# Optimization experiments

Hardware: AMD Instinct MI355X
Metric: run time of the kernel (lower is better)

## Reference

```python
import jax, jax.numpy as jnp
import numpy as np

B, H, W = 32, 64, 64
D = 8        # input_dim (capsule dim of incoming caps)
C = 8        # input_ch (number of incoming capsule types)
DIM = 8      # dim_capsule (output capsule dim)
NCH = 8      # n_channels (number of output capsule types)


def _gconv(x, w, groups, stride=1):
    # x: NHWC, w: HWIO with I = in_ch/groups, O = total out (grouped by output blocks)
    return jax.lax.conv_general_dilated(
        x, w, (stride, stride), 'SAME',
        dimension_numbers=('NHWC', 'HWIO', 'NHWC'),
        feature_group_count=groups)


def setup_inputs():
    key = jax.random.key(0)
    ks = jax.random.split(key, 5)
    inputs = jax.random.normal(ks[0], (B, H, W, D, C), jnp.float32)
    Att_W = jax.random.normal(ks[1], (1, 1, DIM, C, C * NCH), jnp.float32) * 0.05
    ConvTrans_W = jax.random.normal(ks[2], (3, 3, D, C * DIM * NCH), jnp.float32) * 0.05
    ConvTrans_B = jnp.zeros((C * DIM * NCH,), jnp.float32)
    FeaExt_W = jax.random.normal(ks[3], (3, 3, DIM, DIM * NCH), jnp.float32) * 0.05
    FeaExt_B = jnp.zeros((DIM * NCH,), jnp.float32)
    CapsAct_W = jax.random.normal(ks[4], (1, 1, DIM, DIM * NCH), jnp.float32) * 0.05
    CapsAct_B = jnp.zeros((DIM * NCH,), jnp.float32)
    return {'inputs': inputs, 'Att_W': Att_W, 'ConvTrans_W': ConvTrans_W,
            'ConvTrans_B': ConvTrans_B, 'FeaExt_W': FeaExt_W, 'FeaExt_B': FeaExt_B,
            'CapsAct_W': CapsAct_W, 'CapsAct_B': CapsAct_B}


def reference(inputs, Att_W, ConvTrans_W, ConvTrans_B, FeaExt_W, FeaExt_B,
              CapsAct_W, CapsAct_B):
    # --- ConvTrans: per input-capsule-type 3x3 conv (== grouped conv over C groups) ---
    # inputs [B,H,W,D,C] -> [B,H,W,C*D] with group-major ordering
    xt = jnp.transpose(inputs, (0, 1, 2, 4, 3)).reshape(B, H, W, C * D)
    # ConvTrans_W [3,3,D, C*DIM*NCH]: output block i is the kernel for input group i
    y = _gconv(xt, ConvTrans_W, groups=C) + ConvTrans_B  # [B,H,W, C*DIM*NCH]
    # -> u[b,h,w,d,c_in,n]  (matches concat+transpose in the original)
    u = y.reshape(B, H, W, C, DIM, NCH).transpose(0, 1, 2, 4, 3, 5)

    # --- Attention: conv3d with kernel [1,1,DIM,C,C] per output type n (VALID over DIM) ---
    # Att_W [1,1,DIM,C,C*NCH] -> A[d, c_in, n, c_out]
    A = Att_W[0, 0].reshape(DIM, C, NCH, C)
    att = jnp.einsum('bhwdcn,dcno->bhwon', u, A)       # [B,H,W,C,NCH]
    att = jax.nn.softmax(att, axis=3)                  # softmax over input_ch
    v = jnp.einsum('bhwdon,bhwon->bhwdn', u, att)      # weighted sum over input_ch

    # --- FeaExt (3x3, grouped over NCH) + ReLU, then CapsAct (1x1, grouped) ---
    vt = jnp.transpose(v, (0, 1, 2, 4, 3)).reshape(B, H, W, NCH * DIM)
    h1 = jax.nn.relu(_gconv(vt, FeaExt_W, groups=NCH) + FeaExt_B)
    h2 = _gconv(h1, CapsAct_W, groups=NCH) + CapsAct_B
    out = h2.reshape(B, H, W, NCH, DIM).transpose(0, 1, 2, 4, 3)  # [B,H,W,DIM,NCH]
    return out
```

## Files before the change

kernel.cpp:

```cpp
#include <hip/hip_runtime.h>
#include <hip/hip_fp16.h>

#define HH 64
#define WW 64

typedef short bf16x8 __attribute__((ext_vector_type(8)));
typedef float f32x4 __attribute__((ext_vector_type(4)));
typedef unsigned short u16x8 __attribute__((ext_vector_type(8)));

#define FWREP_OFF 0
#define CWREP_OFF 4608
#define LBIAS_OFF 5120
#define M1REP_OFF 5184
#define BUREP_OFF 29760
#define VT_OFF    54336
#define PREP_N    103488

__device__ __forceinline__ unsigned short f2bf(float x) {
  unsigned int u = __float_as_uint(x);
  return (unsigned short)((u + 0x7FFFu + ((u >> 16) & 1u)) >> 16);
}
__device__ __forceinline__ unsigned short f2h(float x) {
  return __half_as_ushort(__float2half(x));
}

union F4H8 { float4 f4; __half h[8]; };

__global__ __launch_bounds__(256) void prep_kernel(
    const float* __restrict__ attw, const float* __restrict__ ctw,
    const float* __restrict__ ctb, const float* __restrict__ few,
    const float* __restrict__ caw, float* __restrict__ ws) {
  int i = blockIdx.x * 256 + threadIdx.x;
  if (i >= PREP_N) return;
  if (i < 4608) {
    int e = i & 63, slot = e >> 3, j = e & 7;
    int k = (i >> 6) % 9, n = i / 576;
    int d = 2 * (slot & 3) + (slot >> 2);
    ws[FWREP_OFF + i] = few[(k * 8 + d) * 64 + n * 8 + j];
  } else if (i < 5120) {
    int z = i - 4608;
    int j = z & 7, d = (z >> 3) & 7, n = (z >> 6) & 7;
    ws[CWREP_OFF + z] = caw[d * 64 + n * 8 + j];
  } else if (i < 5184) {
    int col = i - 5120;
    int s = col >> 4, l15 = col & 15;
    int o = 2 * s + (l15 >> 3), n = l15 & 7;
    float acc = 0.f;
    for (int c = 0; c < 8; ++c)
      for (int d = 0; d < 8; ++d)
        acc += ctb[c * 64 + d * 8 + n] * attw[d * 512 + c * 64 + n * 8 + o];
    ws[LBIAS_OFF + col] = acc;
  } else if (i < 5184 + 49152) {
    int z = i - 5184;
    int j = z & 7, lane = (z >> 3) & 63, s = (z >> 9) & 3;
    int rc = z >> 11, r = rc % 3, c = rc / 3;
    int q = lane >> 4, l15 = lane & 15;
    int t = r * 4 + q, dd = j;
    int o = 2 * s + (l15 >> 3), n = l15 & 7;
    float acc = 0.f;
    if (t < 9)
      for (int d = 0; d < 8; ++d)
        acc += ctw[(t * 8 + dd) * 512 + c * 64 + d * 8 + n] *
               attw[d * 512 + c * 64 + n * 8 + o];
    ((unsigned short*)(ws + M1REP_OFF))[z] = f2bf(acc);
  } else {
    int z = i - 5184 - 49152;
    int j = z & 7, lane = (z >> 3) & 63, s = (z >> 9) & 3;
    int rc = z >> 11, r = rc % 3, c = rc / 3;
    int q = lane >> 4, l15 = lane & 15;
    int t = r * 4 + q, dd = j;
    int d = 2 * s + (l15 >> 3), n = l15 & 7;
    float val = (t < 9) ? ctw[(t * 8 + dd) * 512 + c * 64 + d * 8 + n] : 0.f;
    ((unsigned short*)(ws + BUREP_OFF))[z] = f2bf(val);
  }
}

__global__ __launch_bounds__(256, 2) void caps_stage1(
    const float* __restrict__ in, const float* __restrict__ ws,
    const float* __restrict__ ctb, __half* __restrict__ vt) {
  __shared__ unsigned short xt[181 * 72];
  __shared__ unsigned short attb[128 * 72];
  int bid = blockIdx.x;
  int b = bid >> 5;
  int t5 = bid & 31;
  int ty = t5 >> 3, tx = t5 & 7;
  int tid = threadIdx.x;

  for (int i = tid; i < 181 * 8; i += 256) {
    int c = i & 7, hp = i >> 3;
    float xs[8] = {0.f, 0.f, 0.f, 0.f, 0.f, 0.f, 0.f, 0.f};
    if (hp < 180) {
      int hy = hp / 10, hx = hp - hy * 10;
      int gy = ty * 16 + hy - 1, gx = tx * 8 + hx - 1;
      if (gy >= 0 && gy < HH && gx >= 0 && gx < WW) {
        const float* src = in + (((b * HH + gy) * WW + gx) * 64 + c);
#pragma unroll
        for (int d = 0; d < 8; ++d) xs[d] = src[d * 8];
      }
    }
    u16x8 pk;
#pragma unroll
    for (int d = 0; d < 8; ++d) pk[d] = f2bf(xs[d]);
    *(u16x8*)&xt[hp * 72 + c * 8] = pk;
  }
  __syncthreads();

  int w = __builtin_amdgcn_readfirstlane(tid >> 6);
  int lane = tid & 63;
  int q = lane >> 4, l15 = lane & 15;
  int h = l15 >> 3, n = l15 & 7;

  int hpt[2][3];
#pragma unroll
  for (int i2 = 0; i2 < 2; ++i2) {
    int pyA = (2 * w + i2) * 2 + h;
    int pxA = l15 & 7;
#pragma unroll
    for (int r = 0; r < 3; ++r) {
      int t = r * 4 + q;
      int hp;
      if (t < 9) {
        int ky = t / 3, kx = t - ky * 3;
        hp = (pyA + ky) * 10 + pxA + kx;
      } else {
        hp = 180;
      }
      hpt[i2][r] = hp * 72;
    }
  }

  const bf16x8* m1v = (const bf16x8*)(ws + M1REP_OFF);
  const bf16x8* buv = (const bf16x8*)(ws + BUREP_OFF);
  const float* lb = ws + LBIAS_OFF;

  f32x4 L[2][4];
#pragma unroll
  for (int s = 0; s < 4; ++s) {
    float v0 = lb[s * 16 + l15];
    L[0][s] = (f32x4){v0, v0, v0, v0};
    L[1][s] = (f32x4){v0, v0, v0, v0};
  }
#pragma unroll 1
  for (int c = 0; c < 8; ++c) {
    bf16x8 bm[12];
#pragma unroll
    for (int rs = 0; rs < 12; ++rs) bm[rs] = m1v[(c * 12 + rs) * 64 + lane];
    bf16x8 a[2][3];
#pragma unroll
    for (int i2 = 0; i2 < 2; ++i2)
#pragma unroll
      for (int r = 0; r < 3; ++r)
        a[i2][r] = *(const bf16x8*)&xt[hpt[i2][r] + c * 8];
#pragma unroll
    for (int i2 = 0; i2 < 2; ++i2)
#pragma unroll
      for (int s = 0; s < 4; ++s)
#pragma unroll
        for (int r = 0; r < 3; ++r)
          L[i2][s] = __builtin_amdgcn_mfma_f32_16x16x32_bf16(
              a[i2][r], bm[r * 4 + s], L[i2][s], 0, 0, 0);
  }

#pragma unroll
  for (int i2 = 0; i2 < 2; ++i2) {
    int pbase = (2 * w + i2) * 16 + q * 4;
#pragma unroll
    for (int r = 0; r < 4; ++r) {
      float v0 = L[i2][0][r], v1 = L[i2][1][r], v2 = L[i2][2][r], v3 = L[i2][3][r];
      float pm = fmaxf(fmaxf(v0, v1), fmaxf(v2, v3));
      float m = fmaxf(pm, __shfl_xor(pm, 8));
      float e0 = __expf(v0 - m), e1 = __expf(v1 - m);
      float e2 = __expf(v2 - m), e3 = __expf(v3 - m);
      float ps = e0 + e1 + e2 + e3;
      float inv = 1.f / (ps + __shfl_xor(ps, 8));
      int ab = (pbase + r) * 72 + n * 8 + h;
      attb[ab + 0] = f2h(e0 * inv);
      attb[ab + 2] = f2h(e1 * inv);
      attb[ab + 4] = f2h(e2 * inv);
      attb[ab + 6] = f2h(e3 * inv);
    }
  }
  __syncthreads();

  u16x8 atp[2][4];
#pragma unroll
  for (int i2 = 0; i2 < 2; ++i2)
#pragma unroll
    for (int r = 0; r < 4; ++r)
      atp[i2][r] = *(const u16x8*)&attb[((2 * w + i2) * 16 + q * 4 + r) * 72 + n * 8];

  f32x4 V[2][4];
#pragma unroll
  for (int s = 0; s < 4; ++s) {
    V[0][s] = (f32x4){0.f, 0.f, 0.f, 0.f};
    V[1][s] = (f32x4){0.f, 0.f, 0.f, 0.f};
  }
#pragma unroll 1
  for (int c = 0; c < 8; ++c) {
    bf16x8 bu[12];
#pragma unroll
    for (int rs = 0; rs < 12; ++rs) bu[rs] = buv[(c * 12 + rs) * 64 + lane];
    bf16x8 a[2][3];
#pragma unroll
    for (int i2 = 0; i2 < 2; ++i2)
#pragma unroll
      for (int r = 0; r < 3; ++r)
        a[i2][r] = *(const bf16x8*)&xt[hpt[i2][r] + c * 8];
    f32x4 U[2][4];
#pragma unroll
    for (int s = 0; s < 4; ++s) {
      float bv = ctb[c * 64 + s * 16 + l15];
      U[0][s] = (f32x4){bv, bv, bv, bv};
      U[1][s] = (f32x4){bv, bv, bv, bv};
    }
#pragma unroll
    for (int i2 = 0; i2 < 2; ++i2)
#pragma unroll
      for (int s = 0; s < 4; ++s)
#pragma unroll
        for (int r = 0; r < 3; ++r)
          U[i2][s] = __builtin_amdgcn_mfma_f32_16x16x32_bf16(
              a[i2][r], bu[r * 4 + s], U[i2][s], 0, 0, 0);
#pragma unroll
    for (int i2 = 0; i2 < 2; ++i2)
#pragma unroll
      for (int r = 0; r < 4; ++r) {
        float af = __half2float(__ushort_as_half(atp[i2][r][c]));
#pragma unroll
        for (int s = 0; s < 4; ++s) V[i2][s][r] += U[i2][s][r] * af;
      }
  }

#pragma unroll
  for (int i2 = 0; i2 < 2; ++i2)
#pragma unroll
    for (int r = 0; r < 4; ++r) {
      int p = (2 * w + i2) * 16 + q * 4 + r;
      int gy = ty * 16 + (p >> 3), gx = tx * 8 + (p & 7);
      size_t gp = (size_t)((b * HH + gy) * WW + gx);
      short4 st;
      st.x = (short)f2h(V[i2][0][r]);
      st.y = (short)f2h(V[i2][1][r]);
      st.z = (short)f2h(V[i2][2][r]);
      st.w = (short)f2h(V[i2][3][r]);
      *(short4*)((char*)vt + gp * 128 + n * 16 + h * 8) = st;
    }
}

__global__ __launch_bounds__(512, 6) void caps_stage2(
    const __half* __restrict__ vt, const float* __restrict__ ws,
    const float* __restrict__ fb, const float* __restrict__ cab,
    float* __restrict__ out) {
  __shared__ float smem[64 * 68];
  int bid = blockIdx.x;
  int b = bid >> 6;
  int t = bid & 63;
  int ty = t >> 3, tx = t & 7;
  int y0 = ty * 8 - 1, x0 = tx * 8 - 1;
  int tid = threadIdx.x;

  float4* ht = (float4*)smem;
  for (int i = tid; i < 800; i += 512) {
    int p = i >> 3, q = i & 7;
    int py = p / 10, px = p % 10;
    int gy = y0 + py, gx = x0 + px;
    float4 val = make_float4(0.f, 0.f, 0.f, 0.f);
    if (gy >= 0 && gy < HH && gx >= 0 && gx < WW)
      val = ((const float4*)(vt + ((b * HH + gy) * WW + gx) * 64))[q];
    ht[p * 8 + ((q + p) & 7)] = val;
  }
  __syncthreads();

  int n = __builtin_amdgcn_readfirstlane(tid >> 6);
  int lane = tid & 63;
  int py = lane >> 3, px = lane & 7;
  int p0 = py * 10 + px;
  const float* fwrep = ws + FWREP_OFF;
  const float* cwrep = ws + CWREP_OFF;

  float h1[8];
#pragma unroll
  for (int j = 0; j < 8; ++j) h1[j] = fb[n * 8 + j];

#pragma unroll 1
  for (int k = 0; k < 9; ++k) {
    int kh = k / 3, kw = k % 3;
    int pk = p0 + kh * 10 + kw;
    const float* wp = fwrep + (n * 9 + k) * 64;
    F4H8 xu;
    xu.f4 = ht[pk * 8 + ((n + pk) & 7)];
#pragma unroll
    for (int d = 0; d < 8; ++d) {
      float xv = __half2float(xu.h[d]);
#pragma unroll
      for (int j = 0; j < 8; ++j)
        h1[j] = fmaf(xv, wp[d * 8 + j], h1[j]);
    }
  }
#pragma unroll
  for (int j = 0; j < 8; ++j) h1[j] = fmaxf(h1[j], 0.f);

  float h2[8];
#pragma unroll
  for (int j = 0; j < 8; ++j) h2[j] = cab[n * 8 + j];
#pragma unroll
  for (int d = 0; d < 8; ++d)
#pragma unroll
    for (int j = 0; j < 8; ++j)
      h2[j] = fmaf(h1[d], cwrep[n * 64 + d * 8 + j], h2[j]);

  __syncthreads();
#pragma unroll
  for (int j = 0; j < 8; ++j) {
    int mch = 2 * j + (n >> 2);
    smem[lane * 64 + ((mch + lane) & 15) * 4 + (n & 3)] = h2[j];
  }
  __syncthreads();

  for (int s = tid; s < 1024; s += 512) {
    int p = s >> 4, q = s & 15;
    float4 val = *(float4*)&smem[p * 64 + ((q + p) & 15) * 4];
    int gp = ((b * HH + ty * 8 + (p >> 3)) * WW + tx * 8 + (p & 7));
    *(float4*)(out + gp * 64 + q * 4) = val;
  }
}

extern "C" void kernel_launch(void* const* d_in, const int* in_sizes, int n_in,
                              void* d_out, int out_size, void* d_ws, size_t ws_size,
                              hipStream_t stream) {
  const float* inputs = (const float*)d_in[0];
  const float* attw   = (const float*)d_in[1];
  const float* ctw    = (const float*)d_in[2];
  const float* ctb    = (const float*)d_in[3];
  const float* few    = (const float*)d_in[4];
  const float* fb     = (const float*)d_in[5];
  const float* caw    = (const float*)d_in[6];
  const float* cab    = (const float*)d_in[7];
  float* out = (float*)d_out;
  float* ws  = (float*)d_ws;
  __half* vt = (__half*)(ws + VT_OFF);

  prep_kernel<<<(PREP_N + 255) / 256, 256, 0, stream>>>(attw, ctw, ctb, few, caw, ws);
  caps_stage1<<<32 * 32, 256, 0, stream>>>(inputs, ws, ctb, vt);
  caps_stage2<<<32 * 64, 512, 0, stream>>>(vt, ws, fb, cab, out);
}
```

Baseline: 152.2 us.

## Move stage2 convs onto f16 MFMA and keep softmax weights in registers

```diff
diff --git a/kernel.cpp b/kernel.cpp
--- a/kernel.cpp
+++ b/kernel.cpp
@@ -1,30 +1,22 @@
 #include <hip/hip_runtime.h>
-#include <hip/hip_fp16.h>
 
 #define HH 64
 #define WW 64
 
-typedef short bf16x8 __attribute__((ext_vector_type(8)));
+typedef _Float16 f16;
+typedef f16 f16x8 __attribute__((ext_vector_type(8)));
+typedef f16 f16x4 __attribute__((ext_vector_type(4)));
+typedef f16 f16x2 __attribute__((ext_vector_type(2)));
 typedef float f32x4 __attribute__((ext_vector_type(4)));
-typedef unsigned short u16x8 __attribute__((ext_vector_type(8)));
-
-#define FWREP_OFF 0
-#define CWREP_OFF 4608
-#define LBIAS_OFF 5120
-#define M1REP_OFF 5184
-#define BUREP_OFF 29760
-#define VT_OFF    54336
-#define PREP_N    103488
-
-__device__ __forceinline__ unsigned short f2bf(float x) {
-  unsigned int u = __float_as_uint(x);
-  return (unsigned short)((u + 0x7FFFu + ((u >> 16) & 1u)) >> 16);
-}
-__device__ __forceinline__ unsigned short f2h(float x) {
-  return __half_as_ushort(__float2half(x));
-}
-
-union F4H8 { float4 f4; __half h[8]; };
+
+#define M1_H 0
+#define BU_H 49152
+#define BF_H 98304
+#define BC_H 110592
+#define VT_H 114688
+#define PREP_N (64 + 114688)
+
+union U2 { f16x2 v; int i; };
 
 __global__ __launch_bounds__(256) void prep_kernel(
     const float* __restrict__ attw, const float* __restrict__ ctw,
@@ -32,57 +24,70 @@
     const float* __restrict__ caw, float* __restrict__ ws) {
   int i = blockIdx.x * 256 + threadIdx.x;
   if (i >= PREP_N) return;
-  if (i < 4608) {
-    int e = i & 63, slot = e >> 3, j = e & 7;
-    int k = (i >> 6) % 9, n = i / 576;
-    int d = 2 * (slot & 3) + (slot >> 2);
-    ws[FWREP_OFF + i] = few[(k * 8 + d) * 64 + n * 8 + j];
-  } else if (i < 5120) {
-    int z = i - 4608;
-    int j = z & 7, d = (z >> 3) & 7, n = (z >> 6) & 7;
-    ws[CWREP_OFF + z] = caw[d * 64 + n * 8 + j];
-  } else if (i < 5184) {
-    int col = i - 5120;
-    int s = col >> 4, l15 = col & 15;
+  f16* hb = (f16*)(ws + 64);
+  if (i < 64) {
+    int s = i >> 4, l15 = i & 15;
     int o = 2 * s + (l15 >> 3), n = l15 & 7;
     float acc = 0.f;
     for (int c = 0; c < 8; ++c)
       for (int d = 0; d < 8; ++d)
         acc += ctb[c * 64 + d * 8 + n] * attw[d * 512 + c * 64 + n * 8 + o];
-    ws[LBIAS_OFF + col] = acc;
-  } else if (i < 5184 + 49152) {
-    int z = i - 5184;
-    int j = z & 7, lane = (z >> 3) & 63, s = (z >> 9) & 3;
-    int rc = z >> 11, r = rc % 3, c = rc / 3;
+    ws[i] = acc;
+    return;
+  }
+  int z = i - 64;
+  if (z < BU_H) {
+    int j = z & 7, lane = (z >> 3) & 63, rest = z >> 9;
+    int rs = rest % 12, c = rest / 12;
+    int r = rs >> 2, s = rs & 3;
     int q = lane >> 4, l15 = lane & 15;
-    int t = r * 4 + q, dd = j;
+    int t = r * 4 + q;
     int o = 2 * s + (l15 >> 3), n = l15 & 7;
     float acc = 0.f;
     if (t < 9)
       for (int d = 0; d < 8; ++d)
-        acc += ctw[(t * 8 + dd) * 512 + c * 64 + d * 8 + n] *
+        acc += ctw[(t * 8 + j) * 512 + c * 64 + d * 8 + n] *
                attw[d * 512 + c * 64 + n * 8 + o];
-    ((unsigned short*)(ws + M1REP_OFF))[z] = f2bf(acc);
-  } else {
-    int z = i - 5184 - 49152;
-    int j = z & 7, lane = (z >> 3) & 63, s = (z >> 9) & 3;
-    int rc = z >> 11, r = rc % 3, c = rc / 3;
+    hb[M1_H + z] = (f16)acc;
+  } else if (z < BF_H) {
+    int z2 = z - BU_H;
+    int j = z2 & 7, lane = (z2 >> 3) & 63, rest = z2 >> 9;
+    int rs = rest % 12, c = rest / 12;
+    int r = rs >> 2, s = rs & 3;
     int q = lane >> 4, l15 = lane & 15;
-    int t = r * 4 + q, dd = j;
+    int t = r * 4 + q;
     int d = 2 * s + (l15 >> 3), n = l15 & 7;
-    float val = (t < 9) ? ctw[(t * 8 + dd) * 512 + c * 64 + d * 8 + n] : 0.f;
-    ((unsigned short*)(ws + BUREP_OFF))[z] = f2bf(val);
+    float v = (t < 9) ? ctw[(t * 8 + j) * 512 + c * 64 + d * 8 + n] : 0.f;
+    hb[z] = (f16)v;
+  } else if (z < BC_H) {
+    int z2 = z - BF_H;
+    int j = z2 & 7, lane = (z2 >> 3) & 63, rest = z2 >> 9;
+    int r = rest % 3, g = rest / 3;
+    int q = lane >> 4, l15 = lane & 15;
+    int t = r * 4 + q;
+    int d = 2 * (j & 3) + (j >> 2);
+    float v = 0.f;
+    if (t < 9 && ((l15 >> 3) == (g & 1)))
+      v = few[(t * 8 + d) * 64 + g * 8 + (l15 & 7)];
+    hb[z] = (f16)v;
+  } else if (z < VT_H) {
+    int z2 = z - BC_H;
+    int j = z2 & 7, lane = (z2 >> 3) & 63, rest = z2 >> 9;
+    int s = rest & 3, c2 = rest >> 2;
+    int q = lane >> 4, l15 = lane & 15;
+    int nk = c2 * 4 + q;
+    int nc = 2 * s + (l15 >> 3);
+    float v = (nk == nc) ? caw[j * 64 + nc * 8 + (l15 & 7)] : 0.f;
+    hb[z] = (f16)v;
   }
 }
 
-__global__ __launch_bounds__(256, 2) void caps_stage1(
+__global__ __launch_bounds__(256, 4) void caps_stage1(
     const float* __restrict__ in, const float* __restrict__ ws,
-    const float* __restrict__ ctb, __half* __restrict__ vt) {
-  __shared__ unsigned short xt[181 * 72];
-  __shared__ unsigned short attb[128 * 72];
+    const float* __restrict__ ctb, f16* __restrict__ vt) {
+  __shared__ f16 xt[181 * 72];
   int bid = blockIdx.x;
-  int b = bid >> 5;
-  int t5 = bid & 31;
+  int b = bid >> 5, t5 = bid & 31;
   int ty = t5 >> 3, tx = t5 & 7;
   int tid = threadIdx.x;
 
@@ -98,10 +103,10 @@
         for (int d = 0; d < 8; ++d) xs[d] = src[d * 8];
       }
     }
-    u16x8 pk;
-#pragma unroll
-    for (int d = 0; d < 8; ++d) pk[d] = f2bf(xs[d]);
-    *(u16x8*)&xt[hp * 72 + c * 8] = pk;
+    f16x8 pk;
+#pragma unroll
+    for (int d = 0; d < 8; ++d) pk[d] = (f16)xs[d];
+    *(f16x8*)&xt[hp * 72 + c * 8] = pk;
   }
   __syncthreads();
 
@@ -118,20 +123,18 @@
 #pragma unroll
     for (int r = 0; r < 3; ++r) {
       int t = r * 4 + q;
-      int hp;
+      int hp = 180;
       if (t < 9) {
         int ky = t / 3, kx = t - ky * 3;
         hp = (pyA + ky) * 10 + pxA + kx;
-      } else {
-        hp = 180;
       }
       hpt[i2][r] = hp * 72;
     }
   }
 
-  const bf16x8* m1v = (const bf16x8*)(ws + M1REP_OFF);
-  const bf16x8* buv = (const bf16x8*)(ws + BUREP_OFF);
-  const float* lb = ws + LBIAS_OFF;
+  const f16x8* m1v = (const f16x8*)((const f16*)(ws + 64) + M1_H);
+  const f16x8* buv = (const f16x8*)((const f16*)(ws + 64) + BU_H);
+  const float* lb = ws;
 
   f32x4 L[2][4];
 #pragma unroll
@@ -142,28 +145,29 @@
   }
 #pragma unroll 1
   for (int c = 0; c < 8; ++c) {
-    bf16x8 bm[12];
-#pragma unroll
-    for (int rs = 0; rs < 12; ++rs) bm[rs] = m1v[(c * 12 + rs) * 64 + lane];
-    bf16x8 a[2][3];
+    f16x8 a2[2][3];
 #pragma unroll
     for (int i2 = 0; i2 < 2; ++i2)
 #pragma unroll
       for (int r = 0; r < 3; ++r)
-        a[i2][r] = *(const bf16x8*)&xt[hpt[i2][r] + c * 8];
-#pragma unroll
-    for (int i2 = 0; i2 < 2; ++i2)
-#pragma unroll
-      for (int s = 0; s < 4; ++s)
+        a2[i2][r] = *(const f16x8*)&xt[hpt[i2][r] + c * 8];
+#pragma unroll
+    for (int s = 0; s < 4; ++s) {
+      f16x8 bm[3];
+#pragma unroll
+      for (int r = 0; r < 3; ++r) bm[r] = m1v[(c * 12 + r * 4 + s) * 64 + lane];
+#pragma unroll
+      for (int i2 = 0; i2 < 2; ++i2)
 #pragma unroll
         for (int r = 0; r < 3; ++r)
-          L[i2][s] = __builtin_amdgcn_mfma_f32_16x16x32_bf16(
-              a[i2][r], bm[r * 4 + s], L[i2][s], 0, 0, 0);
-  }
-
-#pragma unroll
-  for (int i2 = 0; i2 < 2; ++i2) {
-    int pbase = (2 * w + i2) * 16 + q * 4;
+          L[i2][s] = __builtin_amdgcn_mfma_f32_16x16x32_f16(
+              a2[i2][r], bm[r], L[i2][s], 0, 0, 0);
+    }
+  }
+
+  f16x2 P[2][4][4];
+#pragma unroll
+  for (int i2 = 0; i2 < 2; ++i2)
 #pragma unroll
     for (int r = 0; r < 4; ++r) {
       float v0 = L[i2][0][r], v1 = L[i2][1][r], v2 = L[i2][2][r], v3 = L[i2][3][r];
@@ -173,21 +177,18 @@
       float e2 = __expf(v2 - m), e3 = __expf(v3 - m);
       float ps = e0 + e1 + e2 + e3;
       float inv = 1.f / (ps + __shfl_xor(ps, 8));
-      int ab = (pbase + r) * 72 + n * 8 + h;
-      attb[ab + 0] = f2h(e0 * inv);
-      attb[ab + 2] = f2h(e1 * inv);
-      attb[ab + 4] = f2h(e2 * inv);
-      attb[ab + 6] = f2h(e3 * inv);
-    }
-  }
-  __syncthreads();
-
-  u16x8 atp[2][4];
-#pragma unroll
-  for (int i2 = 0; i2 < 2; ++i2)
-#pragma unroll
-    for (int r = 0; r < 4; ++r)
-      atp[i2][r] = *(const u16x8*)&attb[((2 * w + i2) * 16 + q * 4 + r) * 72 + n * 8];
+      f16 o0 = (f16)(e0 * inv), o1 = (f16)(e1 * inv);
+      f16 o2 = (f16)(e2 * inv), o3 = (f16)(e3 * inv);
+      U2 p01, p23, r01, r23;
+      p01.v = (f16x2){o0, o1};
+      p23.v = (f16x2){o2, o3};
+      r01.i = __shfl_xor(p01.i, 8);
+      r23.i = __shfl_xor(p23.i, 8);
+      P[i2][r][0] = h ? (f16x2){r01.v[0], o0} : (f16x2){o0, r01.v[0]};
+      P[i2][r][1] = h ? (f16x2){r01.v[1], o1} : (f16x2){o1, r01.v[1]};
+      P[i2][r][2] = h ? (f16x2){r23.v[0], o2} : (f16x2){o2, r23.v[0]};
+      P[i2][r][3] = h ? (f16x2){r23.v[1], o3} : (f16x2){o3, r23.v[1]};
+    }
 
   f32x4 V[2][4];
 #pragma unroll
@@ -195,133 +196,185 @@
     V[0][s] = (f32x4){0.f, 0.f, 0.f, 0.f};
     V[1][s] = (f32x4){0.f, 0.f, 0.f, 0.f};
   }
-#pragma unroll 1
+#pragma unroll
   for (int c = 0; c < 8; ++c) {
-    bf16x8 bu[12];
-#pragma unroll
-    for (int rs = 0; rs < 12; ++rs) bu[rs] = buv[(c * 12 + rs) * 64 + lane];
-    bf16x8 a[2][3];
+    f16x8 a2[2][3];
 #pragma unroll
     for (int i2 = 0; i2 < 2; ++i2)
 #pragma unroll
       for (int r = 0; r < 3; ++r)
-        a[i2][r] = *(const bf16x8*)&xt[hpt[i2][r] + c * 8];
-    f32x4 U[2][4];
+        a2[i2][r] = *(const f16x8*)&xt[hpt[i2][r] + c * 8];
+    float attf[2][4];
+#pragma unroll
+    for (int i2 = 0; i2 < 2; ++i2)
+#pragma unroll
+      for (int r = 0; r < 4; ++r)
+        attf[i2][r] = (float)P[i2][r][c >> 1][c & 1];
 #pragma unroll
     for (int s = 0; s < 4; ++s) {
+      f16x8 bu[3];
+#pragma unroll
+      for (int r = 0; r < 3; ++r) bu[r] = buv[(c * 12 + r * 4 + s) * 64 + lane];
       float bv = ctb[c * 64 + s * 16 + l15];
-      U[0][s] = (f32x4){bv, bv, bv, bv};
-      U[1][s] = (f32x4){bv, bv, bv, bv};
-    }
-#pragma unroll
-    for (int i2 = 0; i2 < 2; ++i2)
-#pragma unroll
-      for (int s = 0; s < 4; ++s)
+#pragma unroll
+      for (int i2 = 0; i2 < 2; ++i2) {
+        f32x4 U = (f32x4){bv, bv, bv, bv};
 #pragma unroll
         for (int r = 0; r < 3; ++r)
-          U[i2][s] = __builtin_amdgcn_mfma_f32_16x16x32_bf16(
-              a[i2][r], bu[r * 4 + s], U[i2][s], 0, 0, 0);
-#pragma unroll
-    for (int i2 = 0; i2 < 2; ++i2)
-#pragma unroll
-      for (int r = 0; r < 4; ++r) {
-        float af = __half2float(__ushort_as_half(atp[i2][r][c]));
-#pragma unroll
-        for (int s = 0; s < 4; ++s) V[i2][s][r] += U[i2][s][r] * af;
-      }
-  }
-
+          U = __builtin_amdgcn_mfma_f32_16x16x32_f16(a2[i2][r], bu[r], U, 0, 0, 0);
+#pragma unroll
+        for (int r = 0; r < 4; ++r) V[i2][s][r] += U[r] * attf[i2][r];
+      }
+    }
+  }
+
+  __syncthreads();
+  f16* vtmp = xt;
 #pragma unroll
   for (int i2 = 0; i2 < 2; ++i2)
 #pragma unroll
     for (int r = 0; r < 4; ++r) {
       int p = (2 * w + i2) * 16 + q * 4 + r;
-      int gy = ty * 16 + (p >> 3), gx = tx * 8 + (p & 7);
-      size_t gp = (size_t)((b * HH + gy) * WW + gx);
-      short4 st;
-      st.x = (short)f2h(V[i2][0][r]);
-      st.y = (short)f2h(V[i2][1][r]);
-      st.z = (short)f2h(V[i2][2][r]);
-      st.w = (short)f2h(V[i2][3][r]);
-      *(short4*)((char*)vt + gp * 128 + n * 16 + h * 8) = st;
-    }
+      f16x4 st;
+#pragma unroll
+      for (int s = 0; s < 4; ++s) st[s] = (f16)V[i2][s][r];
+      *(f16x4*)&vtmp[p * 72 + n * 8 + h * 4] = st;
+    }
+  __syncthreads();
+  for (int idx = tid; idx < 1024; idx += 256) {
+    int p = idx >> 3, q2 = idx & 7;
+    float4 val = *(float4*)&vtmp[p * 72 + q2 * 8];
+    int gy = ty * 16 + (p >> 3), gx = tx * 8 + (p & 7);
+    ((float4*)(vt + ((b * HH + gy) * WW + gx) * 64))[q2] = val;
+  }
 }
 
-__global__ __launch_bounds__(512, 6) void caps_stage2(
-    const __half* __restrict__ vt, const float* __restrict__ ws,
+__global__ __launch_bounds__(256, 4) void caps_stage2(
+    const f16* __restrict__ vt, const float* __restrict__ ws,
     const float* __restrict__ fb, const float* __restrict__ cab,
     float* __restrict__ out) {
-  __shared__ float smem[64 * 68];
+  __shared__ float smemf[8704];
+  f16* vtile = (f16*)smemf;
   int bid = blockIdx.x;
-  int b = bid >> 6;
-  int t = bid & 63;
-  int ty = t >> 3, tx = t & 7;
-  int y0 = ty * 8 - 1, x0 = tx * 8 - 1;
+  int b = bid >> 5, t5 = bid & 31;
+  int ty = t5 >> 3, tx = t5 & 7;
   int tid = threadIdx.x;
 
-  float4* ht = (float4*)smem;
-  for (int i = tid; i < 800; i += 512) {
-    int p = i >> 3, q = i & 7;
-    int py = p / 10, px = p % 10;
-    int gy = y0 + py, gx = x0 + px;
+  for (int i = tid; i < 181 * 8; i += 256) {
+    int q2 = i & 7, hp = i >> 3;
     float4 val = make_float4(0.f, 0.f, 0.f, 0.f);
-    if (gy >= 0 && gy < HH && gx >= 0 && gx < WW)
-      val = ((const float4*)(vt + ((b * HH + gy) * WW + gx) * 64))[q];
-    ht[p * 8 + ((q + p) & 7)] = val;
-  }
-  __syncthreads();
-
-  int n = __builtin_amdgcn_readfirstlane(tid >> 6);
+    if (hp < 180) {
+      int hy = hp / 10, hx = hp - hy * 10;
+      int gy = ty * 16 + hy - 1, gx = tx * 8 + hx - 1;
+      if (gy >= 0 && gy < HH && gx >= 0 && gx < WW)
+        val = ((const float4*)(vt + ((b * HH + gy) * WW + gx) * 64))[q2];
+    }
+    *(float4*)&vtile[hp * 72 + q2 * 8] = val;
+  }
+  __syncthreads();
+
+  int w = __builtin_amdgcn_readfirstlane(tid >> 6);
   int lane = tid & 63;
-  int py = lane >> 3, px = lane & 7;
-  int p0 = py * 10 + px;
-  const float* fwrep = ws + FWREP_OFF;
-  const float* cwrep = ws + CWREP_OFF;
-
-  float h1[8];
-#pragma unroll
-  for (int j = 0; j < 8; ++j) h1[j] = fb[n * 8 + j];
-
-#pragma unroll 1
-  for (int k = 0; k < 9; ++k) {
-    int kh = k / 3, kw = k % 3;
-    int pk = p0 + kh * 10 + kw;
-    const float* wp = fwrep + (n * 9 + k) * 64;
-    F4H8 xu;
-    xu.f4 = ht[pk * 8 + ((n + pk) & 7)];
-#pragma unroll
-    for (int d = 0; d < 8; ++d) {
-      float xv = __half2float(xu.h[d]);
-#pragma unroll
-      for (int j = 0; j < 8; ++j)
-        h1[j] = fmaf(xv, wp[d * 8 + j], h1[j]);
-    }
-  }
-#pragma unroll
-  for (int j = 0; j < 8; ++j) h1[j] = fmaxf(h1[j], 0.f);
-
-  float h2[8];
-#pragma unroll
-  for (int j = 0; j < 8; ++j) h2[j] = cab[n * 8 + j];
-#pragma unroll
-  for (int d = 0; d < 8; ++d)
-#pragma unroll
-    for (int j = 0; j < 8; ++j)
-      h2[j] = fmaf(h1[d], cwrep[n * 64 + d * 8 + j], h2[j]);
-
-  __syncthreads();
-#pragma unroll
-  for (int j = 0; j < 8; ++j) {
-    int mch = 2 * j + (n >> 2);
-    smem[lane * 64 + ((mch + lane) & 15) * 4 + (n & 3)] = h2[j];
-  }
-  __syncthreads();
-
-  for (int s = tid; s < 1024; s += 512) {
-    int p = s >> 4, q = s & 15;
-    float4 val = *(float4*)&smem[p * 64 + ((q + p) & 15) * 4];
-    int gp = ((b * HH + ty * 8 + (p >> 3)) * WW + tx * 8 + (p & 7));
-    *(float4*)(out + gp * 64 + q * 4) = val;
+  int q = lane >> 4, l15 = lane & 15;
+  int h = l15 >> 3, j7 = l15 & 7;
+
+  int hpt[2][3];
+#pragma unroll
+  for (int i2 = 0; i2 < 2; ++i2) {
+    int pyA = (2 * w + i2) * 2 + h;
+#pragma unroll
+    for (int r = 0; r < 3; ++r) {
+      int t = r * 4 + q;
+      int hp = 180;
+      if (t < 9) {
+        int ky = t / 3, kx = t - ky * 3;
+        hp = (pyA + ky) * 10 + j7 + kx;
+      }
+      hpt[i2][r] = hp * 72;
+    }
+  }
+
+  const f16x8* bfv = (const f16x8*)((const f16*)(ws + 64) + BF_H);
+  const f16x8* bcv = (const f16x8*)((const f16*)(ws + 64) + BC_H);
+
+  f32x4 L[2][4];
+#pragma unroll
+  for (int s = 0; s < 4; ++s) {
+    float bvv = fb[(2 * s + h) * 8 + j7];
+    L[0][s] = (f32x4){bvv, bvv, bvv, bvv};
+    L[1][s] = (f32x4){bvv, bvv, bvv, bvv};
+  }
+#pragma unroll
+  for (int g = 0; g < 8; ++g) {
+    int sg = g >> 1;
+#pragma unroll
+    for (int r = 0; r < 3; ++r) {
+      f16x8 bf = bfv[(g * 3 + r) * 64 + lane];
+#pragma unroll
+      for (int i2 = 0; i2 < 2; ++i2) {
+        f16x8 a = *(const f16x8*)&vtile[hpt[i2][r] + g * 8];
+        L[i2][sg] = __builtin_amdgcn_mfma_f32_16x16x32_f16(a, bf, L[i2][sg], 0, 0, 0);
+      }
+    }
+  }
+#pragma unroll
+  for (int i2 = 0; i2 < 2; ++i2)
+#pragma unroll
+    for (int s = 0; s < 4; ++s)
+#pragma unroll
+      for (int r = 0; r < 4; ++r) L[i2][s][r] = fmaxf(L[i2][s][r], 0.f);
+
+  __syncthreads();
+  f16* h1t = (f16*)smemf;
+#pragma unroll
+  for (int i2 = 0; i2 < 2; ++i2)
+#pragma unroll
+    for (int s = 0; s < 4; ++s)
+#pragma unroll
+      for (int r = 0; r < 4; ++r)
+        h1t[((2 * w + i2) * 16 + q * 4 + r) * 72 + (2 * s + h) * 8 + j7] =
+            (f16)L[i2][s][r];
+  __syncthreads();
+
+  f32x4 H[2][4];
+#pragma unroll
+  for (int s = 0; s < 4; ++s) {
+    float bvv = cab[(2 * s + h) * 8 + j7];
+    H[0][s] = (f32x4){bvv, bvv, bvv, bvv};
+    H[1][s] = (f32x4){bvv, bvv, bvv, bvv};
+  }
+#pragma unroll
+  for (int c2 = 0; c2 < 2; ++c2) {
+    f16x8 a2[2];
+#pragma unroll
+    for (int i2 = 0; i2 < 2; ++i2)
+      a2[i2] = *(const f16x8*)&h1t[((2 * w + i2) * 16 + l15) * 72 + c2 * 32 + q * 8];
+#pragma unroll
+    for (int s = 0; s < 4; ++s) {
+      f16x8 bc = bcv[(c2 * 4 + s) * 64 + lane];
+#pragma unroll
+      for (int i2 = 0; i2 < 2; ++i2)
+        H[i2][s] = __builtin_amdgcn_mfma_f32_16x16x32_f16(a2[i2], bc, H[i2][s], 0, 0, 0);
+    }
+  }
+
+  __syncthreads();
+  float* outbuf = smemf;
+#pragma unroll
+  for (int i2 = 0; i2 < 2; ++i2)
+#pragma unroll
+    for (int s = 0; s < 4; ++s)
+#pragma unroll
+      for (int r = 0; r < 4; ++r)
+        outbuf[((2 * w + i2) * 16 + q * 4 + r) * 68 + j7 * 8 + 2 * s + h] =
+            H[i2][s][r];
+  __syncthreads();
+
+  for (int idx = tid; idx < 2048; idx += 256) {
+    int p = idx >> 4, q4 = idx & 15;
+    float4 val = *(float4*)&outbuf[p * 68 + q4 * 4];
+    int gy = ty * 16 + (p >> 3), gx = tx * 8 + (p & 7);
+    *(float4*)(out + ((b * HH + gy) * WW + gx) * 64 + q4 * 4) = val;
   }
 }
 
@@ -338,9 +391,9 @@
   const float* cab    = (const float*)d_in[7];
   float* out = (float*)d_out;
   float* ws  = (float*)d_ws;
-  __half* vt = (__half*)(ws + VT_OFF);
+  f16* vt = (f16*)(ws + 64) + VT_H;
 
   prep_kernel<<<(PREP_N + 255) / 256, 256, 0, stream>>>(attw, ctw, ctb, few, caw, ws);
   caps_stage1<<<32 * 32, 256, 0, stream>>>(inputs, ws, ctb, vt);
-  caps_stage2<<<32 * 64, 512, 0, stream>>>(vt, ws, fb, cab, out);
+  caps_stage2<<<32 * 32, 256, 0, stream>>>(vt, ws, fb, cab, out);
 }
```

Measured after the change: 264.5 us. +73.8%, slower.
